# Optimization experiments

Measured on AMD Instinct MI355X. Metric: run time of the kernel, lower is better.

The kernel has to match this reference:

```python
import jax, jax.numpy as jnp
import numpy as np

N_NODES = 65536
N_EDGES = 1048576
F_IN = 64
F_OUT = 128
K = 3


def setup_inputs() -> dict:
    key = jax.random.key(0)
    k1, k2, k3, k4, k5 = jax.random.split(key, 5)
    X = jax.random.normal(k1, (N_NODES, F_IN), dtype=jnp.float32)
    edge_row = jax.random.randint(k2, (N_EDGES,), 0, N_NODES, dtype=jnp.int32)
    edge_col = jax.random.randint(k3, (N_EDGES,), 0, N_NODES, dtype=jnp.int32)
    # rescaled-Laplacian values; scale down so the K-step recurrence stays bounded
    edge_val = jax.random.normal(k4, (N_EDGES,), dtype=jnp.float32) * 0.05
    W = jax.random.normal(k5, (F_IN * K, F_OUT), dtype=jnp.float32) * (1.0 / np.sqrt(F_IN * K))
    b = jnp.zeros((F_OUT,), dtype=jnp.float32)
    return {"X": X, "edge_row": edge_row, "edge_col": edge_col,
            "edge_val": edge_val, "W": W, "b": b}


def reference(X, edge_row, edge_col, edge_val, W, b):
    # Sparse L @ Y via gather + segment-sum over COO edges (irregular access).
    N = X.shape[0]

    def spmm(Y):
        # [E, F] gathered messages, scattered back to rows
        msgs = edge_val[:, None] * Y[edge_col]
        return jax.ops.segment_sum(msgs, edge_row, num_segments=N)

    # Chebyshev recurrence: T0 = X, T1 = L X, T_k = 2 L T_{k-1} - T_{k-2}
    T_prev2 = X
    T_prev1 = spmm(X)
    terms = [T_prev2, T_prev1]
    for _ in range(2, K):
        T_next = 2.0 * spmm(T_prev1) - T_prev2
        terms.append(T_next)
        T_prev2, T_prev1 = T_prev1, T_next

    H = jnp.concatenate(terms[:K], axis=-1)  # [N, K*Fin]
    # Linear; dropout is identity at eval / p=0
    return H @ W + b
```

## Files before the change

### kernel.cpp

```cpp
#include <hip/hip_runtime.h>

#define N_NODES 65536
#define N_EDGES 1048576
#define F_IN 64
#define F_OUT 128
#define KDIM (F_IN * 3)
#define NB 1024


__global__ __launch_bounds__(256) void zero_bcur(int* __restrict__ bcur)
{
    ((int4*)bcur)[threadIdx.x] = make_int4(0, 0, 0, 0);
}

__global__ __launch_bounds__(256) void bucket_hist(const int* __restrict__ erow,
                                                   int* __restrict__ bcur)
{
    __shared__ int h[NB];
    int t = threadIdx.x;
    for (int i = t; i < NB; i += 256) h[i] = 0;
    __syncthreads();
    int base = blockIdx.x * 8192;
    for (int j = 0; j < 8; ++j) {
        int4 r = *(const int4*)(erow + base + j * 1024 + t * 4);
        atomicAdd(&h[r.x >> 6], 1);
        atomicAdd(&h[r.y >> 6], 1);
        atomicAdd(&h[r.z >> 6], 1);
        atomicAdd(&h[r.w >> 6], 1);
    }
    __syncthreads();
    for (int i = t; i < NB; i += 256)
        if (h[i]) atomicAdd(&bcur[i], h[i]);
}

__global__ __launch_bounds__(256) void scan_buckets(int* __restrict__ bcur,
                                                    int* __restrict__ boff)
{
    __shared__ int s[256];
    int t = threadIdx.x;
    int4 c = ((const int4*)bcur)[t];
    int tsum = c.x + c.y + c.z + c.w;
    s[t] = tsum;
    __syncthreads();
    for (int d = 1; d < 256; d <<= 1) {
        int v = (t >= d) ? s[t - d] : 0;
        __syncthreads();
        s[t] += v;
        __syncthreads();
    }
    int run = s[t] - tsum;
    int4 o;
    o.x = run;
    o.y = o.x + c.x;
    o.z = o.y + c.y;
    o.w = o.z + c.z;
    ((int4*)boff)[t] = o;
    ((int4*)bcur)[t] = o;
    if (t == 255) boff[NB] = N_EDGES;
}

__global__ __launch_bounds__(256) void bucketize(
    const int* __restrict__ erow, const int* __restrict__ ecol,
    const float* __restrict__ eval, int* __restrict__ bcur,
    const int* __restrict__ boff_unused, int2* __restrict__ bent)
{
    __shared__ int h[NB];
    __shared__ int gbase[NB];
    int t = threadIdx.x;
    for (int i = t; i < NB; i += 256) h[i] = 0;
    __syncthreads();
    int base = blockIdx.x * 8192;
    for (int j = 0; j < 8; ++j) {
        int4 r = *(const int4*)(erow + base + j * 1024 + t * 4);
        atomicAdd(&h[r.x >> 6], 1);
        atomicAdd(&h[r.y >> 6], 1);
        atomicAdd(&h[r.z >> 6], 1);
        atomicAdd(&h[r.w >> 6], 1);
    }
    __syncthreads();
    for (int i = t; i < NB; i += 256) {
        int cnt = h[i];
        gbase[i] = cnt ? atomicAdd(&bcur[i], cnt) : 0;
        h[i] = 0;
    }
    __syncthreads();
    for (int j = 0; j < 8; ++j) {
        int4   r = *(const int4*)(erow + base + j * 1024 + t * 4);
        int4   c = *(const int4*)(ecol + base + j * 1024 + t * 4);
        float4 v = *(const float4*)(eval + base + j * 1024 + t * 4);
        {
            int b = r.x >> 6; int p = atomicAdd(&h[b], 1);
            bent[gbase[b] + p] = make_int2((int)(((unsigned)r.x << 16) | (unsigned)c.x), __float_as_int(v.x));
        }
        {
            int b = r.y >> 6; int p = atomicAdd(&h[b], 1);
            bent[gbase[b] + p] = make_int2((int)(((unsigned)r.y << 16) | (unsigned)c.y), __float_as_int(v.y));
        }
        {
            int b = r.z >> 6; int p = atomicAdd(&h[b], 1);
            bent[gbase[b] + p] = make_int2((int)(((unsigned)r.z << 16) | (unsigned)c.z), __float_as_int(v.z));
        }
        {
            int b = r.w >> 6; int p = atomicAdd(&h[b], 1);
            bent[gbase[b] + p] = make_int2((int)(((unsigned)r.w << 16) | (unsigned)c.w), __float_as_int(v.w));
        }
    }
}

__global__ __launch_bounds__(256) void build_csr(
    const int* __restrict__ boff, const int2* __restrict__ bent,
    int* __restrict__ off, int2* __restrict__ csr)
{
    __shared__ int rh[64];
    __shared__ int rbase[64];
    int b = blockIdx.x;
    int t = threadIdx.x;
    int s = boff[b];
    int e = boff[b + 1];
    int n = e - s;
    if (t < 64) rh[t] = 0;
    __syncthreads();
    for (int i = t; i < n; i += 256) {
        unsigned rc = (unsigned)bent[s + i].x;
        atomicAdd(&rh[(rc >> 16) & 63], 1);
    }
    __syncthreads();
    if (t == 0) {
        int run = s;
        for (int k = 0; k < 64; ++k) { rbase[k] = run; run += rh[k]; }
    }
    __syncthreads();
    if (t < 64) {
        off[b * 64 + t] = rbase[t];
        rh[t] = 0;
    }
    if (b == NB - 1 && t == 0) off[N_NODES] = N_EDGES;
    __syncthreads();
    for (int i = t; i < n; i += 256) {
        int2 en = bent[s + i];
        unsigned rc = (unsigned)en.x;
        int rl = (rc >> 16) & 63;
        int p = atomicAdd(&rh[rl], 1);
        csr[rbase[rl] + p] = make_int2((int)(rc & 0xFFFFu), en.y);
    }
}

template <int MODE>
__global__ __launch_bounds__(256) void spmm_csr(
    const int* __restrict__ off, const int2* __restrict__ csr,
    const float* __restrict__ Y, const float* __restrict__ X,
    float* __restrict__ out)
{
    int r    = blockIdx.x * 4 + (threadIdx.x >> 6);
    int lane = threadIdx.x & 63;
    int s = off[r];
    int e = off[r + 1];
    float a0 = 0.f, a1 = 0.f, a2 = 0.f, a3 = 0.f;
    int i = s;
    for (; i + 4 <= e; i += 4) {
        int2 e0 = csr[i];
        int2 e1 = csr[i + 1];
        int2 e2 = csr[i + 2];
        int2 e3 = csr[i + 3];
        float y0 = Y[(size_t)e0.x * F_IN + lane];
        float y1 = Y[(size_t)e1.x * F_IN + lane];
        float y2 = Y[(size_t)e2.x * F_IN + lane];
        float y3 = Y[(size_t)e3.x * F_IN + lane];
        a0 = fmaf(__int_as_float(e0.y), y0, a0);
        a1 = fmaf(__int_as_float(e1.y), y1, a1);
        a2 = fmaf(__int_as_float(e2.y), y2, a2);
        a3 = fmaf(__int_as_float(e3.y), y3, a3);
    }
    for (; i < e; ++i) {
        int2 ed = csr[i];
        a0 = fmaf(__int_as_float(ed.y), Y[(size_t)ed.x * F_IN + lane], a0);
    }
    float acc = (a0 + a1) + (a2 + a3);
    size_t o = (size_t)r * F_IN + lane;
    if (MODE == 1) out[o] = acc;
    else           out[o] = 2.f * acc - X[o];
}

__global__ __launch_bounds__(256) void gemm_out(
    const float* __restrict__ X, const float* __restrict__ T1,
    const float* __restrict__ T2, const float* __restrict__ W,
    const float* __restrict__ bias, float* __restrict__ out)
{
    __shared__ float Hs[32][KDIM];
    int t = threadIdx.x;
    int brow = blockIdx.x * 32;

    for (int i = t; i < 32 * 48; i += 256) {
        int r = i / 48;
        int k4 = (i % 48) * 4;
        int gr = brow + r;
        const float* src;
        if (k4 < 64)       src = X  + (size_t)gr * F_IN + k4;
        else if (k4 < 128) src = T1 + (size_t)gr * F_IN + (k4 - 64);
        else               src = T2 + (size_t)gr * F_IN + (k4 - 128);
        *(float4*)&Hs[r][k4] = *(const float4*)src;
    }
    __syncthreads();

    int tc = t & 31;
    int tr = t >> 5;
    float acc[4][4] = {};

    for (int k4 = 0; k4 < KDIM; k4 += 4) {
        float4 w0 = *(const float4*)(W + (size_t)(k4 + 0) * F_OUT + tc * 4);
        float4 w1 = *(const float4*)(W + (size_t)(k4 + 1) * F_OUT + tc * 4);
        float4 w2 = *(const float4*)(W + (size_t)(k4 + 2) * F_OUT + tc * 4);
        float4 w3 = *(const float4*)(W + (size_t)(k4 + 3) * F_OUT + tc * 4);
        #pragma unroll
        for (int rr = 0; rr < 4; ++rr) {
            float4 h = *(const float4*)&Hs[tr + rr * 8][k4];
            acc[rr][0] = fmaf(h.x, w0.x, acc[rr][0]);
            acc[rr][1] = fmaf(h.x, w0.y, acc[rr][1]);
            acc[rr][2] = fmaf(h.x, w0.z, acc[rr][2]);
            acc[rr][3] = fmaf(h.x, w0.w, acc[rr][3]);
            acc[rr][0] = fmaf(h.y, w1.x, acc[rr][0]);
            acc[rr][1] = fmaf(h.y, w1.y, acc[rr][1]);
            acc[rr][2] = fmaf(h.y, w1.z, acc[rr][2]);
            acc[rr][3] = fmaf(h.y, w1.w, acc[rr][3]);
            acc[rr][0] = fmaf(h.z, w2.x, acc[rr][0]);
            acc[rr][1] = fmaf(h.z, w2.y, acc[rr][1]);
            acc[rr][2] = fmaf(h.z, w2.z, acc[rr][2]);
            acc[rr][3] = fmaf(h.z, w2.w, acc[rr][3]);
            acc[rr][0] = fmaf(h.w, w3.x, acc[rr][0]);
            acc[rr][1] = fmaf(h.w, w3.y, acc[rr][1]);
            acc[rr][2] = fmaf(h.w, w3.z, acc[rr][2]);
            acc[rr][3] = fmaf(h.w, w3.w, acc[rr][3]);
        }
    }

    float4 bb = *(const float4*)(bias + tc * 4);
    #pragma unroll
    for (int rr = 0; rr < 4; ++rr) {
        int gr = brow + tr + rr * 8;
        float4 o;
        o.x = acc[rr][0] + bb.x;
        o.y = acc[rr][1] + bb.y;
        o.z = acc[rr][2] + bb.z;
        o.w = acc[rr][3] + bb.w;
        *(float4*)(out + (size_t)gr * F_OUT + tc * 4) = o;
    }
}

extern "C" void kernel_launch(void* const* d_in, const int* in_sizes, int n_in,
                              void* d_out, int out_size, void* d_ws, size_t ws_size,
                              hipStream_t stream)
{
    const float* X    = (const float*)d_in[0];
    const int*   erow = (const int*)  d_in[1];
    const int*   ecol = (const int*)  d_in[2];
    const float* eval = (const float*)d_in[3];
    const float* W    = (const float*)d_in[4];
    const float* bias = (const float*)d_in[5];
    float* out = (float*)d_out;

    float* T1 = (float*)d_ws;
    float* T2 = T1 + (size_t)N_NODES * F_IN;

    int*  off  = (int*)d_out;
    int2* csr  = (int2*)(off + 65600);
    int*  boff = (int*)(csr + N_EDGES);
    int*  bcur = boff + 1088;
    int2* bent = (int2*)(bcur + 1024);

    zero_bcur<<<1, 256, 0, stream>>>(bcur);
    bucket_hist<<<128, 256, 0, stream>>>(erow, bcur);
    scan_buckets<<<1, 256, 0, stream>>>(bcur, boff);
    bucketize<<<128, 256, 0, stream>>>(erow, ecol, eval, bcur, boff, bent);
    build_csr<<<NB, 256, 0, stream>>>(boff, bent, off, csr);

    spmm_csr<1><<<N_NODES / 4, 256, 0, stream>>>(off, csr, X, X, T1);
    spmm_csr<2><<<N_NODES / 4, 256, 0, stream>>>(off, csr, T1, X, T2);

    gemm_out<<<N_NODES / 32, 256, 0, stream>>>(X, T1, T2, W, bias, out);
}
```

Measured before the change: 267.0 us.

## Store Chebyshev terms in bf16 and compute output GEMM with MFMA

Converts X and the intermediate T1/T2 terms to bf16, so the SpMM gathers read half the bytes while still accumulating in fp32. The final dense projection is replaced with a bf16 MFMA 16x16x32 kernel that uses a pre-packed, swizzled W held in LDS. This cuts gather bandwidth and FP32 ALU work in the GEMM. In exchange it adds two small conversion kernels and loses precision to bf16 rounding, which may hurt accuracy against the fp32 reference.

```diff
diff --git a/kernel.cpp b/kernel.cpp
--- a/kernel.cpp
+++ b/kernel.cpp
@@ -6,6 +6,46 @@
 #define F_OUT 128
 #define KDIM (F_IN * 3)
 #define NB 1024
+
+typedef float f32x4 __attribute__((ext_vector_type(4)));
+typedef short bf16x8 __attribute__((ext_vector_type(8)));
+
+static __device__ __forceinline__ unsigned short f2bf(float f)
+{
+    unsigned u = __float_as_uint(f);
+    u += 0x7FFFu + ((u >> 16) & 1u);
+    return (unsigned short)(u >> 16);
+}
+static __device__ __forceinline__ float bf2f(unsigned short h)
+{
+    return __uint_as_float((unsigned)h << 16);
+}
+
+
+__global__ __launch_bounds__(256) void wpack(const float* __restrict__ W,
+                                             unsigned short* __restrict__ Wp)
+{
+    int p = blockIdx.x * 256 + threadIdx.x;
+    int j   = p & 7;
+    int gx  = (p >> 3) & 3;
+    int c15 = (p >> 5) & 15;
+    int n   = (p >> 9) & 7;
+    int kk  = p >> 12;
+    int g   = gx ^ (c15 & 3);
+    int k   = kk * 32 + g * 8 + j;
+    int c   = n * 16 + c15;
+    Wp[p] = f2bf(W[k * F_OUT + c]);
+}
+
+__global__ __launch_bounds__(256) void xconvert(const float* __restrict__ X,
+                                                unsigned short* __restrict__ Xb)
+{
+    unsigned i = (blockIdx.x * 256u + threadIdx.x) * 4u;
+    float4 x = *(const float4*)(X + i);
+    ushort4 o;
+    o.x = f2bf(x.x); o.y = f2bf(x.y); o.z = f2bf(x.z); o.w = f2bf(x.w);
+    *(ushort4*)(Xb + i) = o;
+}
 
 
 __global__ __launch_bounds__(256) void zero_bcur(int* __restrict__ bcur)
@@ -62,7 +102,7 @@
 __global__ __launch_bounds__(256) void bucketize(
     const int* __restrict__ erow, const int* __restrict__ ecol,
     const float* __restrict__ eval, int* __restrict__ bcur,
-    const int* __restrict__ boff_unused, int2* __restrict__ bent)
+    int2* __restrict__ bent)
 {
     __shared__ int h[NB];
     __shared__ int gbase[NB];
@@ -146,10 +186,10 @@
 }
 
 template <int MODE>
-__global__ __launch_bounds__(256) void spmm_csr(
+__global__ __launch_bounds__(256) void spmm_b(
     const int* __restrict__ off, const int2* __restrict__ csr,
-    const float* __restrict__ Y, const float* __restrict__ X,
-    float* __restrict__ out)
+    const unsigned short* __restrict__ Yb, const float* __restrict__ X,
+    unsigned short* __restrict__ outb)
 {
     int r    = blockIdx.x * 4 + (threadIdx.x >> 6);
     int lane = threadIdx.x & 63;
@@ -162,10 +202,10 @@
         int2 e1 = csr[i + 1];
         int2 e2 = csr[i + 2];
         int2 e3 = csr[i + 3];
-        float y0 = Y[(size_t)e0.x * F_IN + lane];
-        float y1 = Y[(size_t)e1.x * F_IN + lane];
-        float y2 = Y[(size_t)e2.x * F_IN + lane];
-        float y3 = Y[(size_t)e3.x * F_IN + lane];
+        float y0 = bf2f(Yb[(size_t)e0.x * F_IN + lane]);
+        float y1 = bf2f(Yb[(size_t)e1.x * F_IN + lane]);
+        float y2 = bf2f(Yb[(size_t)e2.x * F_IN + lane]);
+        float y3 = bf2f(Yb[(size_t)e3.x * F_IN + lane]);
         a0 = fmaf(__int_as_float(e0.y), y0, a0);
         a1 = fmaf(__int_as_float(e1.y), y1, a1);
         a2 = fmaf(__int_as_float(e2.y), y2, a2);
@@ -173,76 +213,63 @@
     }
     for (; i < e; ++i) {
         int2 ed = csr[i];
-        a0 = fmaf(__int_as_float(ed.y), Y[(size_t)ed.x * F_IN + lane], a0);
+        a0 = fmaf(__int_as_float(ed.y), bf2f(Yb[(size_t)ed.x * F_IN + lane]), a0);
     }
     float acc = (a0 + a1) + (a2 + a3);
     size_t o = (size_t)r * F_IN + lane;
-    if (MODE == 1) out[o] = acc;
-    else           out[o] = 2.f * acc - X[o];
-}
-
-__global__ __launch_bounds__(256) void gemm_out(
-    const float* __restrict__ X, const float* __restrict__ T1,
-    const float* __restrict__ T2, const float* __restrict__ W,
+    if (MODE == 2) acc = 2.f * acc - X[o];
+    outb[o] = f2bf(acc);
+}
+
+__global__ __launch_bounds__(512) void gemm_mfma(
+    const unsigned short* __restrict__ Xb, const unsigned short* __restrict__ T1b,
+    const unsigned short* __restrict__ T2b, const unsigned short* __restrict__ Wp,
     const float* __restrict__ bias, float* __restrict__ out)
 {
-    __shared__ float Hs[32][KDIM];
-    int t = threadIdx.x;
-    int brow = blockIdx.x * 32;
-
-    for (int i = t; i < 32 * 48; i += 256) {
-        int r = i / 48;
-        int k4 = (i % 48) * 4;
-        int gr = brow + r;
-        const float* src;
-        if (k4 < 64)       src = X  + (size_t)gr * F_IN + k4;
-        else if (k4 < 128) src = T1 + (size_t)gr * F_IN + (k4 - 64);
-        else               src = T2 + (size_t)gr * F_IN + (k4 - 128);
-        *(float4*)&Hs[r][k4] = *(const float4*)src;
-    }
-    __syncthreads();
-
-    int tc = t & 31;
-    int tr = t >> 5;
-    float acc[4][4] = {};
-
-    for (int k4 = 0; k4 < KDIM; k4 += 4) {
-        float4 w0 = *(const float4*)(W + (size_t)(k4 + 0) * F_OUT + tc * 4);
-        float4 w1 = *(const float4*)(W + (size_t)(k4 + 1) * F_OUT + tc * 4);
-        float4 w2 = *(const float4*)(W + (size_t)(k4 + 2) * F_OUT + tc * 4);
-        float4 w3 = *(const float4*)(W + (size_t)(k4 + 3) * F_OUT + tc * 4);
+    __shared__ __align__(16) unsigned short Wl[24576];
+    int t = threadIdx.x;
+    for (int i = t; i < 3072; i += 512)
+        ((float4*)Wl)[i] = ((const float4*)Wp)[i];
+    __syncthreads();
+
+    int w   = t >> 6;
+    int l   = t & 63;
+    int c15 = l & 15;
+    int g   = l >> 4;
+    int brow = blockIdx.x * 128 + w * 16;
+    int arow = brow + c15;
+
+    const unsigned short* srcs[3] = {Xb, T1b, T2b};
+    bf16x8 a[6];
+    #pragma unroll
+    for (int kk = 0; kk < 6; ++kk) {
+        const unsigned short* src = srcs[kk >> 1];
+        a[kk] = *(const bf16x8*)(src + (size_t)arow * F_IN + (kk & 1) * 32 + g * 8);
+    }
+
+    f32x4 acc[8];
+    #pragma unroll
+    for (int n = 0; n < 8; ++n) acc[n] = (f32x4){0.f, 0.f, 0.f, 0.f};
+
+    int gx = g ^ (c15 & 3);
+    #pragma unroll
+    for (int kk = 0; kk < 6; ++kk) {
         #pragma unroll
-        for (int rr = 0; rr < 4; ++rr) {
-            float4 h = *(const float4*)&Hs[tr + rr * 8][k4];
-            acc[rr][0] = fmaf(h.x, w0.x, acc[rr][0]);
-            acc[rr][1] = fmaf(h.x, w0.y, acc[rr][1]);
-            acc[rr][2] = fmaf(h.x, w0.z, acc[rr][2]);
-            acc[rr][3] = fmaf(h.x, w0.w, acc[rr][3]);
-            acc[rr][0] = fmaf(h.y, w1.x, acc[rr][0]);
-            acc[rr][1] = fmaf(h.y, w1.y, acc[rr][1]);
-            acc[rr][2] = fmaf(h.y, w1.z, acc[rr][2]);
-            acc[rr][3] = fmaf(h.y, w1.w, acc[rr][3]);
-            acc[rr][0] = fmaf(h.z, w2.x, acc[rr][0]);
-            acc[rr][1] = fmaf(h.z, w2.y, acc[rr][1]);
-            acc[rr][2] = fmaf(h.z, w2.z, acc[rr][2]);
-            acc[rr][3] = fmaf(h.z, w2.w, acc[rr][3]);
-            acc[rr][0] = fmaf(h.w, w3.x, acc[rr][0]);
-            acc[rr][1] = fmaf(h.w, w3.y, acc[rr][1]);
-            acc[rr][2] = fmaf(h.w, w3.z, acc[rr][2]);
-            acc[rr][3] = fmaf(h.w, w3.w, acc[rr][3]);
-        }
-    }
-
-    float4 bb = *(const float4*)(bias + tc * 4);
+        for (int n = 0; n < 8; ++n) {
+            int idx = (((kk * 8 + n) * 16 + c15) * 4 + gx) * 8;
+            bf16x8 b = *(const bf16x8*)&Wl[idx];
+            acc[n] = __builtin_amdgcn_mfma_f32_16x16x32_bf16(a[kk], b, acc[n], 0, 0, 0);
+        }
+    }
+
     #pragma unroll
-    for (int rr = 0; rr < 4; ++rr) {
-        int gr = brow + tr + rr * 8;
-        float4 o;
-        o.x = acc[rr][0] + bb.x;
-        o.y = acc[rr][1] + bb.y;
-        o.z = acc[rr][2] + bb.z;
-        o.w = acc[rr][3] + bb.w;
-        *(float4*)(out + (size_t)gr * F_OUT + tc * 4) = o;
+    for (int n = 0; n < 8; ++n) {
+        float bv = bias[n * 16 + c15];
+        #pragma unroll
+        for (int r = 0; r < 4; ++r) {
+            int orow = brow + g * 4 + r;
+            out[(size_t)orow * F_OUT + n * 16 + c15] = acc[n][r] + bv;
+        }
     }
 }
 
@@ -258,8 +285,10 @@
     const float* bias = (const float*)d_in[5];
     float* out = (float*)d_out;
 
-    float* T1 = (float*)d_ws;
-    float* T2 = T1 + (size_t)N_NODES * F_IN;
+    unsigned short* Xb  = (unsigned short*)d_ws;
+    unsigned short* T1b = Xb  + (size_t)N_NODES * F_IN;
+    unsigned short* T2b = T1b + (size_t)N_NODES * F_IN;
+    unsigned short* Wp  = T2b + (size_t)N_NODES * F_IN;
 
     int*  off  = (int*)d_out;
     int2* csr  = (int2*)(off + 65600);
@@ -267,14 +296,17 @@
     int*  bcur = boff + 1088;
     int2* bent = (int2*)(bcur + 1024);
 
+    wpack<<<96, 256, 0, stream>>>(W, Wp);
+    xconvert<<<N_NODES * F_IN / 4 / 256, 256, 0, stream>>>(X, Xb);
+
     zero_bcur<<<1, 256, 0, stream>>>(bcur);
     bucket_hist<<<128, 256, 0, stream>>>(erow, bcur);
     scan_buckets<<<1, 256, 0, stream>>>(bcur, boff);
-    bucketize<<<128, 256, 0, stream>>>(erow, ecol, eval, bcur, boff, bent);
+    bucketize<<<128, 256, 0, stream>>>(erow, ecol, eval, bcur, bent);
     build_csr<<<NB, 256, 0, stream>>>(boff, bent, off, csr);
 
-    spmm_csr<1><<<N_NODES / 4, 256, 0, stream>>>(off, csr, X, X, T1);
-    spmm_csr<2><<<N_NODES / 4, 256, 0, stream>>>(off, csr, T1, X, T2);
-
-    gemm_out<<<N_NODES / 32, 256, 0, stream>>>(X, T1, T2, W, bias, out);
-}
+    spmm_b<1><<<N_NODES / 4, 256, 0, stream>>>(off, csr, Xb, X, T1b);
+    spmm_b<2><<<N_NODES / 4, 256, 0, stream>>>(off, csr, T1b, X, T2b);
+
+    gemm_mfma<<<N_NODES / 128, 512, 0, stream>>>(Xb, T1b, T2b, Wp, bias, out);
+}
```

Result: faster. 218.2 us (-18.3%).
